# Kernel optimization log

Hardware: AMD Instinct MI355X
Metric: run time of the kernel (lower is better)

Reference implementation:

```python
import jax, jax.numpy as jnp
import numpy as np

NEG_INF = -jnp.inf


def setup_inputs() -> dict:
    key = jax.random.key(0)
    ks = jax.random.split(key, 6)
    B, S, D, DK = 8, 2048, 1024, 128
    x = jax.random.normal(ks[0], (B, S, D), dtype=jnp.float32)
    context = jax.random.normal(ks[1], (B, S, D), dtype=jnp.float32)
    # torch nn.Linear weights: [out_features, in_features]
    Wq = jax.random.normal(ks[2], (DK, D), dtype=jnp.float32) * 0.02
    Wk = jax.random.normal(ks[3], (DK, D), dtype=jnp.float32) * 0.02
    Wv = jax.random.normal(ks[4], (DK, D), dtype=jnp.float32) * 0.02
    # valid lengths in [S//2, S] so every row has at least one valid key
    batch_lengths = jax.random.randint(ks[5], (B,), S // 2, S + 1, dtype=jnp.int32)
    return {
        "x": x,
        "context": context,
        "Wq": Wq,
        "Wk": Wk,
        "Wv": Wv,
        "batch_lengths": batch_lengths,
        "max_len": S,
        "decoding": 1,
    }


def reference(x, context, Wq, Wk, Wv, batch_lengths, max_len, decoding):
    B, S, D = x.shape
    dk = Wq.shape[0]
    pos = jnp.arange(S)
    # outputMask: 1.0 for t < length, else 0.0; broadcast over feature dim dk
    valid = pos[None, :] < batch_lengths[:, None]            # [B, S]
    mask = valid[:, :, None].astype(x.dtype)                 # [B, S, 1] (broadcast to dk)
    Q = jnp.einsum('bsd,kd->bsk', context, Wq) * mask        # [B, S, dk]
    K = jnp.einsum('bsd,kd->bsk', context, Wk) * mask
    V = jnp.einsum('bsd,kd->bsk', x, Wv) * mask
    energy = jnp.einsum('bqk,bjk->bqj', Q, K)                # [B, S, S]
    # attnMask: -inf at padded key positions (j >= length)
    key_pad = ~valid                                         # [B, S]
    energy = jnp.where(key_pad[:, None, :], NEG_INF, energy)
    if decoding:
        # causal: energy[:, i, j] = -inf for j > i (the python double loop)
        causal = pos[:, None] < pos[None, :]                 # [S, S], True above diag
        energy = jnp.where(causal[None, :, :], NEG_INF, energy)
    score = jax.nn.softmax(energy / jnp.sqrt(jnp.asarray(dk, x.dtype)), axis=-1)
    return jnp.einsum('bqj,bjk->bqk', score, V)              # [B, S, dk]
```

## Files before the change

kernel.cpp:

```cpp
#include <hip/hip_runtime.h>
#include <hip/hip_bf16.h>

#define BB 8
#define SS 2048
#define DD 1024
#define DKK 128

using bf16x8  = __attribute__((ext_vector_type(8))) __bf16;
using floatx4 = __attribute__((ext_vector_type(4))) float;
using intx4   = __attribute__((ext_vector_type(4))) int;

__device__ __forceinline__ void lds16(const void* g, void* l) {
    __builtin_amdgcn_global_load_lds((const __attribute__((address_space(1))) void*)g,
                                     (__attribute__((address_space(3))) void*)l, 16, 0, 0);
}

__device__ __forceinline__ int pack2(float a, float b) {
    union { __bf16 h; unsigned short u; } ua, ub;
    ua.h = (__bf16)a; ub.h = (__bf16)b;
    return (int)(ua.u | ((unsigned)ub.u << 16));
}

__global__ __launch_bounds__(256) void convw_kernel(
    const float* __restrict__ Wq, const float* __restrict__ Wk,
    const float* __restrict__ Wv, __bf16* __restrict__ Wt)
{
    const int z = blockIdx.y;
    const float* W = (z == 0) ? Wq : (z == 1) ? Wk : Wv;
    const int t  = blockIdx.x * 256 + threadIdx.x;
    const int n  = t >> 7;
    const int k0 = (t & 127) * 8;
    float4 f0 = *(const float4*)(W + n * DD + k0);
    float4 f1 = *(const float4*)(W + n * DD + k0 + 4);
    bf16x8 v;
    v[0]=(__bf16)f0.x; v[1]=(__bf16)f0.y; v[2]=(__bf16)f0.z; v[3]=(__bf16)f0.w;
    v[4]=(__bf16)f1.x; v[5]=(__bf16)f1.y; v[6]=(__bf16)f1.z; v[7]=(__bf16)f1.w;
    const int kb  = (k0 >> 3) & 7;
    const int kbs = kb ^ (n & 7);
    *(bf16x8*)(Wt + (size_t)z * 131072 + ((k0 >> 6) * 128 + n) * 64 + kbs * 8) = v;
}

__global__ __launch_bounds__(256, 2) void proj_kernel(
    const float* __restrict__ x, const float* __restrict__ ctx,
    const __bf16* __restrict__ Wt, const int* __restrict__ lengths,
    __bf16* __restrict__ Qb, __bf16* __restrict__ Kb, __bf16* __restrict__ Vt)
{
    __shared__ __align__(16) __bf16 SH[20992];
    __bf16* Abuf = SH;
    __bf16* Wl0  = SH + 4608;
    __bf16* Wl1  = SH + 12800;
    __bf16* T    = SH + 4608;

    const int isV = blockIdx.x >= 256;
    const int m0  = (isV ? blockIdx.x - 256 : blockIdx.x) * 64;
    const int b   = m0 >> 11;
    const int s0  = m0 & (SS - 1);
    const int len = lengths[b];
    if (s0 >= len) return;

    const int tid  = threadIdx.x;
    const int wave = tid >> 6;
    const int lane = tid & 63;
    const int quad = lane >> 4;
    const int l16  = lane & 15;
    const int wm   = wave >> 1;
    const int wn   = wave & 1;

    const float*  A  = isV ? x : ctx;
    const __bf16* W0 = isV ? (Wt + 262144) : Wt;
    const __bf16* W1 = Wt + 131072;

    const int r    = tid >> 2;
    const int kseg = (tid & 3) * 16;
    const float* Ab = A + (size_t)(m0 + r) * DD + kseg;

    floatx4 acc[2][2][4];
#pragma unroll
    for (int m_ = 0; m_ < 2; ++m_)
#pragma unroll
        for (int i = 0; i < 2; ++i)
#pragma unroll
            for (int j = 0; j < 4; ++j) acc[m_][i][j] = (floatx4){0.f,0.f,0.f,0.f};

    float4 pf[4];
#pragma unroll
    for (int i = 0; i < 4; ++i) pf[i] = *(const float4*)(Ab + i * 4);

    for (int t = 0; t < 16; ++t) {
        __syncthreads();
        {
            bf16x8 c0, c1;
            c0[0]=(__bf16)pf[0].x; c0[1]=(__bf16)pf[0].y; c0[2]=(__bf16)pf[0].z; c0[3]=(__bf16)pf[0].w;
            c0[4]=(__bf16)pf[1].x; c0[5]=(__bf16)pf[1].y; c0[6]=(__bf16)pf[1].z; c0[7]=(__bf16)pf[1].w;
            c1[0]=(__bf16)pf[2].x; c1[1]=(__bf16)pf[2].y; c1[2]=(__bf16)pf[2].z; c1[3]=(__bf16)pf[2].w;
            c1[4]=(__bf16)pf[3].x; c1[5]=(__bf16)pf[3].y; c1[6]=(__bf16)pf[3].z; c1[7]=(__bf16)pf[3].w;
            *(bf16x8*)&Abuf[r * 72 + kseg]     = c0;
            *(bf16x8*)&Abuf[r * 72 + kseg + 8] = c1;
        }
#pragma unroll
        for (int i = 0; i < 4; ++i) {
            const int c = wave * 4 + i;
            lds16(W0 + (size_t)t * 8192 + c * 512 + lane * 8, Wl0 + c * 512);
            if (!isV)
                lds16(W1 + (size_t)t * 8192 + c * 512 + lane * 8, Wl1 + c * 512);
        }
        if (t < 15) {
            const float* ap = Ab + (t + 1) * 64;
#pragma unroll
            for (int i = 0; i < 4; ++i) pf[i] = *(const float4*)(ap + i * 4);
        }
        __syncthreads();

#pragma unroll
        for (int kh = 0; kh < 2; ++kh) {
            bf16x8 af[2];
#pragma unroll
            for (int mt = 0; mt < 2; ++mt)
                af[mt] = *(const bf16x8*)&Abuf[(wm*32 + mt*16 + l16) * 72 + kh*32 + quad*8];
            const int kb = kh * 4 + quad;
#pragma unroll
            for (int nt = 0; nt < 4; ++nt) {
                const int n = wn * 64 + nt * 16 + l16;
                const int off = n * 64 + ((kb ^ (n & 7)) << 3);
                bf16x8 w0 = *(const bf16x8*)&Wl0[off];
#pragma unroll
                for (int mt = 0; mt < 2; ++mt)
                    acc[0][mt][nt] = __builtin_amdgcn_mfma_f32_16x16x32_bf16(af[mt], w0, acc[0][mt][nt], 0, 0, 0);
                if (!isV) {
                    bf16x8 w1 = *(const bf16x8*)&Wl1[off];
#pragma unroll
                    for (int mt = 0; mt < 2; ++mt)
                        acc[1][mt][nt] = __builtin_amdgcn_mfma_f32_16x16x32_bf16(af[mt], w1, acc[1][mt][nt], 0, 0, 0);
                }
            }
        }
    }

    if (!isV) {
#pragma unroll
        for (int mt = 0; mt < 2; ++mt)
#pragma unroll
            for (int rr = 0; rr < 4; ++rr) {
                const int row = m0 + wm*32 + mt*16 + quad*4 + rr;
                const float mk = ((row & (SS - 1)) < len) ? 1.f : 0.f;
#pragma unroll
                for (int nt = 0; nt < 4; ++nt) {
                    const int col = wn*64 + nt*16 + l16;
                    Qb[(size_t)row * DKK + col] = (__bf16)(acc[0][mt][nt][rr] * mk);
                    Kb[(size_t)row * DKK + col] = (__bf16)(acc[1][mt][nt][rr] * mk);
                }
            }
    } else {
        __syncthreads();
#pragma unroll
        for (int mt = 0; mt < 2; ++mt)
#pragma unroll
            for (int nt = 0; nt < 4; ++nt)
#pragma unroll
                for (int rr = 0; rr < 4; ++rr) {
                    const int s = wm*32 + mt*16 + quad*4 + rr;
                    const int n = wn*64 + nt*16 + l16;
                    const float mk = (s0 + s < len) ? 1.f : 0.f;
                    T[n * 72 + s] = (__bf16)(acc[0][mt][nt][rr] * mk);
                }
        __syncthreads();
        const int n = tid >> 1, h = tid & 1;
        __bf16* dst = Vt + (size_t)b * DKK * SS + (size_t)n * SS + s0 + h * 32;
#pragma unroll
        for (int i = 0; i < 4; ++i)
            *(bf16x8*)(dst + i * 8) = *(const bf16x8*)&T[n * 72 + h * 32 + i * 8];
    }
}

__global__ __launch_bounds__(256) void vmean_kernel(
    const __bf16* __restrict__ Vt, const int* __restrict__ lengths,
    float* __restrict__ Vmean)
{
    const int b   = blockIdx.x >> 3;
    const int g3  = blockIdx.x & 7;
    const int len = lengths[b];
    const int tid = threadIdx.x;
    const int n   = g3 * 16 + (tid >> 4);
    const int sl  = (tid & 15) * 128;
    const __bf16* src = Vt + (size_t)b * DKK * SS + (size_t)n * SS + sl;
    float s = 0.f;
#pragma unroll
    for (int i = 0; i < 16; ++i) {
        bf16x8 v = *(const bf16x8*)(src + i * 8);
#pragma unroll
        for (int j = 0; j < 8; ++j)
            s += (sl + i * 8 + j < len) ? (float)v[j] : 0.f;
    }
#pragma unroll
    for (int off = 1; off < 16; off <<= 1)
        s += __shfl_xor(s, off, 64);
    if ((tid & 15) == 0) Vmean[b * DKK + n] = s / (float)len;
}

__global__ __launch_bounds__(64) void attn_kernel(
    const __bf16* __restrict__ Qb, const __bf16* __restrict__ Kb,
    const __bf16* __restrict__ Vt, const int* __restrict__ lengths,
    const float* __restrict__ Vmean, float* __restrict__ out)
{
    const int b    = blockIdx.x & 7;
    const int t    = 127 - (blockIdx.x >> 3);
    const int qw   = t * 16;
    const int len  = lengths[b];
    const int lane = threadIdx.x;
    const int quad = lane >> 4;
    const int l16  = lane & 15;

    if (qw >= len) {
        const float4 v0 = *(const float4*)(Vmean + b * DKK + l16 * 8);
        const float4 v1 = *(const float4*)(Vmean + b * DKK + l16 * 8 + 4);
#pragma unroll
        for (int rr = 0; rr < 4; ++rr) {
            float* p = out + (size_t)(b * SS + qw + quad * 4 + rr) * DKK + l16 * 8;
            *(float4*)p = v0; *(float4*)(p + 4) = v1;
        }
        return;
    }

    const int jmax = min(qw + 16, len);
    const __bf16* Qbase = Qb + (size_t)(b * SS + qw) * DKK;
    const __bf16* Kbase = Kb + (size_t)b * SS * DKK;
    const __bf16* Vbase = Vt + (size_t)b * DKK * SS;

    bf16x8 qfrag[4];
#pragma unroll
    for (int cc = 0; cc < 4; ++cc)
        qfrag[cc] = *(const bf16x8*)(Qbase + (size_t)l16 * DKK + cc * 32 + quad * 8);

    floatx4 oacc[8];
#pragma unroll
    for (int nt = 0; nt < 8; ++nt) oacc[nt] = (floatx4){0.f,0.f,0.f,0.f};
    float lsum = 0.f;
    const float scale = 0.08838834764831845f;
    const int   iq    = qw + l16;

    auto loadK = [&](bf16x8 (&kf)[2][4], int j0) {
#pragma unroll
        for (int jt = 0; jt < 2; ++jt)
#pragma unroll
            for (int cc = 0; cc < 4; ++cc)
                kf[jt][cc] = *(const bf16x8*)(
                    Kbase + (size_t)(j0 + jt*16 + l16) * DKK + cc*32 + quad*8);
    };
    auto process = [&](const bf16x8 (&kf)[2][4], int j0) {
        bf16x8 vf[8];
#pragma unroll
        for (int nt = 0; nt < 8; ++nt)
            vf[nt] = *(const bf16x8*)(Vbase + (size_t)(nt*16 + l16) * SS + j0 + quad*8);

        floatx4 st[2];
#pragma unroll
        for (int jt = 0; jt < 2; ++jt) {
            st[jt] = (floatx4){0.f,0.f,0.f,0.f};
#pragma unroll
            for (int cc = 0; cc < 4; ++cc)
                st[jt] = __builtin_amdgcn_mfma_f32_16x16x32_bf16(
                    kf[jt][cc], qfrag[cc], st[jt], 0, 0, 0);
        }
        int pk[2][2];
#pragma unroll
        for (int jt = 0; jt < 2; ++jt) {
            float p[4];
#pragma unroll
            for (int rr = 0; rr < 4; ++rr) {
                const int j = j0 + jt*16 + quad*4 + rr;
                p[rr] = (j > iq || j >= len) ? 0.f : __expf(st[jt][rr] * scale - 8.f);
                lsum += p[rr];
            }
            pk[jt][0] = pack2(p[0], p[1]);
            pk[jt][1] = pack2(p[2], p[3]);
        }
        const int a0 = (((quad & 1) << 5) + l16) << 2;
        const int a1 = a0 + 64;
        const int r00 = __builtin_amdgcn_ds_bpermute(a0, pk[0][0]);
        const int r01 = __builtin_amdgcn_ds_bpermute(a0, pk[0][1]);
        const int r02 = __builtin_amdgcn_ds_bpermute(a0, pk[1][0]);
        const int r03 = __builtin_amdgcn_ds_bpermute(a0, pk[1][1]);
        const int r10 = __builtin_amdgcn_ds_bpermute(a1, pk[0][0]);
        const int r11 = __builtin_amdgcn_ds_bpermute(a1, pk[0][1]);
        const int r12 = __builtin_amdgcn_ds_bpermute(a1, pk[1][0]);
        const int r13 = __builtin_amdgcn_ds_bpermute(a1, pk[1][1]);
        const bool hi = quad >= 2;
        union { intx4 i; bf16x8 h; } u;
        u.i = (intx4){ hi ? r02 : r00, hi ? r03 : r01,
                       hi ? r12 : r10, hi ? r13 : r11 };
#pragma unroll
        for (int nt = 0; nt < 8; ++nt)
            oacc[nt] = __builtin_amdgcn_mfma_f32_16x16x32_bf16(u.h, vf[nt], oacc[nt], 0, 0, 0);
    };

    bf16x8 kfA[2][4], kfB[2][4];
    loadK(kfA, 0);
    int j0 = 0;
    while (true) {
        bool more = (j0 + 32 < jmax);
        if (more) loadK(kfB, j0 + 32);
        process(kfA, j0);
        j0 += 32;
        if (!more) break;
        more = (j0 + 32 < jmax);
        if (more) loadK(kfA, j0 + 32);
        process(kfB, j0);
        j0 += 32;
        if (!more) break;
    }

    lsum += __shfl_xor(lsum, 16, 64);
    lsum += __shfl_xor(lsum, 32, 64);
    float inv[4];
#pragma unroll
    for (int rr = 0; rr < 4; ++rr)
        inv[rr] = 1.f / __shfl(lsum, quad * 4 + rr, 64);
#pragma unroll
    for (int nt = 0; nt < 8; ++nt)
#pragma unroll
        for (int rr = 0; rr < 4; ++rr)
            out[(size_t)(b * SS + qw + quad*4 + rr) * DKK + nt*16 + l16] =
                oacc[nt][rr] * inv[rr];
}

extern "C" void kernel_launch(void* const* d_in, const int* in_sizes, int n_in,
                              void* d_out, int out_size, void* d_ws, size_t ws_size,
                              hipStream_t stream) {
    const float* x   = (const float*)d_in[0];
    const float* ctx = (const float*)d_in[1];
    const float* Wq  = (const float*)d_in[2];
    const float* Wk  = (const float*)d_in[3];
    const float* Wv  = (const float*)d_in[4];
    const int* lengths = (const int*)d_in[5];
    float* out = (float*)d_out;

    char* ws = (char*)d_ws;
    __bf16* Wt = (__bf16*)ws;
    __bf16* Qb = (__bf16*)(ws + 786432);
    __bf16* Kb = (__bf16*)(ws + 786432 + 4194304);
    __bf16* Vt = (__bf16*)(ws + 786432 + 8388608);
    float*  Vm = (float*) (ws + 786432 + 12582912);

    convw_kernel<<<dim3(64, 3), 256, 0, stream>>>(Wq, Wk, Wv, Wt);
    proj_kernel<<<512, 256, 0, stream>>>(x, ctx, Wt, lengths, Qb, Kb, Vt);
    vmean_kernel<<<64, 256, 0, stream>>>(Vt, lengths, Vm);
    attn_kernel<<<1024, 64, 0, stream>>>(Qb, Kb, Vt, lengths, Vm, out);
}
```

Before: 237.1 us.

## Split attention key loop across four waves with LDS reduction

The attention kernel now launches 256 threads per query tile. Each of the four waves processes an interleaved quarter of the key blocks, stepping by 128. Partial output accumulators and row sums are then reduced through shared memory before normalization and the store. This shortens the per-block serial key loop, which limited the long causal tiles, at the cost of LDS traffic, a barrier and more threads per block.

```diff
diff --git a/kernel.cpp b/kernel.cpp
--- a/kernel.cpp
+++ b/kernel.cpp
@@ -197,27 +197,31 @@
     if ((tid & 15) == 0) Vmean[b * DKK + n] = s / (float)len;
 }
 
-__global__ __launch_bounds__(64) void attn_kernel(
+__global__ __launch_bounds__(256) void attn_kernel(
     const __bf16* __restrict__ Qb, const __bf16* __restrict__ Kb,
     const __bf16* __restrict__ Vt, const int* __restrict__ lengths,
     const float* __restrict__ Vmean, float* __restrict__ out)
 {
+    __shared__ float redO[4][16][132];
+    __shared__ float redL[4][16];
+
     const int b    = blockIdx.x & 7;
     const int t    = 127 - (blockIdx.x >> 3);
     const int qw   = t * 16;
     const int len  = lengths[b];
-    const int lane = threadIdx.x;
+    const int tid  = threadIdx.x;
+    const int wave = tid >> 6;
+    const int lane = tid & 63;
     const int quad = lane >> 4;
     const int l16  = lane & 15;
 
     if (qw >= len) {
-        const float4 v0 = *(const float4*)(Vmean + b * DKK + l16 * 8);
-        const float4 v1 = *(const float4*)(Vmean + b * DKK + l16 * 8 + 4);
-#pragma unroll
-        for (int rr = 0; rr < 4; ++rr) {
-            float* p = out + (size_t)(b * SS + qw + quad * 4 + rr) * DKK + l16 * 8;
-            *(float4*)p = v0; *(float4*)(p + 4) = v1;
-        }
+        const int row = tid >> 4;
+        const int c8  = (tid & 15) * 8;
+        float* op = out + (size_t)(b * SS + qw + row) * DKK + c8;
+        const float4 v0 = *(const float4*)(Vmean + b * DKK + c8);
+        const float4 v1 = *(const float4*)(Vmean + b * DKK + c8 + 4);
+        *(float4*)op = v0; *(float4*)(op + 4) = v1;
         return;
     }
 
@@ -294,33 +298,45 @@
     };
 
     bf16x8 kfA[2][4], kfB[2][4];
-    loadK(kfA, 0);
-    int j0 = 0;
-    while (true) {
-        bool more = (j0 + 32 < jmax);
-        if (more) loadK(kfB, j0 + 32);
-        process(kfA, j0);
-        j0 += 32;
-        if (!more) break;
-        more = (j0 + 32 < jmax);
-        if (more) loadK(kfA, j0 + 32);
-        process(kfB, j0);
-        j0 += 32;
-        if (!more) break;
+    int j0 = wave * 32;
+    if (j0 < jmax) {
+        loadK(kfA, j0);
+        while (true) {
+            bool more = (j0 + 128 < jmax);
+            if (more) loadK(kfB, j0 + 128);
+            process(kfA, j0);
+            j0 += 128;
+            if (!more) break;
+            more = (j0 + 128 < jmax);
+            if (more) loadK(kfA, j0 + 128);
+            process(kfB, j0);
+            j0 += 128;
+            if (!more) break;
+        }
     }
 
     lsum += __shfl_xor(lsum, 16, 64);
     lsum += __shfl_xor(lsum, 32, 64);
-    float inv[4];
-#pragma unroll
-    for (int rr = 0; rr < 4; ++rr)
-        inv[rr] = 1.f / __shfl(lsum, quad * 4 + rr, 64);
+
 #pragma unroll
     for (int nt = 0; nt < 8; ++nt)
 #pragma unroll
         for (int rr = 0; rr < 4; ++rr)
-            out[(size_t)(b * SS + qw + quad*4 + rr) * DKK + nt*16 + l16] =
-                oacc[nt][rr] * inv[rr];
+            redO[wave][quad*4 + rr][nt*16 + l16] = oacc[nt][rr];
+    if (lane < 16) redL[wave][l16] = lsum;
+    __syncthreads();
+
+    const int row = tid >> 4;
+    const int c8  = (tid & 15) * 8;
+    const float lt = redL[0][row] + redL[1][row] + redL[2][row] + redL[3][row];
+    const float inv = 1.f / lt;
+    float* op = out + (size_t)(b * SS + qw + row) * DKK + c8;
+#pragma unroll
+    for (int k = 0; k < 8; ++k) {
+        const float s = redO[0][row][c8+k] + redO[1][row][c8+k]
+                      + redO[2][row][c8+k] + redO[3][row][c8+k];
+        op[k] = s * inv;
+    }
 }
 
 extern "C" void kernel_launch(void* const* d_in, const int* in_sizes, int n_in,
@@ -344,5 +360,5 @@
     convw_kernel<<<dim3(64, 3), 256, 0, stream>>>(Wq, Wk, Wv, Wt);
     proj_kernel<<<512, 256, 0, stream>>>(x, ctx, Wt, lengths, Qb, Kb, Vt);
     vmean_kernel<<<64, 256, 0, stream>>>(Vt, lengths, Vm);
-    attn_kernel<<<1024, 64, 0, stream>>>(Qb, Kb, Vt, lengths, Vm, out);
-}
+    attn_kernel<<<1024, 256, 0, stream>>>(Qb, Kb, Vt, lengths, Vm, out);
+}
```

Result: no change. 234.6 us (-1.1%).

## Share K/V tiles in LDS across four waves of a 64-row query block

Applied to the files above, without the earlier changes.

Attention blocks now hold 4 waves covering 64 query rows. K and V chunks of 64 keys are staged into double-buffered, XOR-swizzled LDS using direct global-to-LDS loads, so four waves reuse each tile instead of each reading K/V from global memory on its own. This cuts redundant global/L2 traffic but adds __syncthreads per chunk and reduces the grid to 256 blocks. Causal work per block is coarser, so some waves compute masked chunks they would have skipped before.

```diff
diff --git a/kernel.cpp b/kernel.cpp
--- a/kernel.cpp
+++ b/kernel.cpp
@@ -197,73 +197,96 @@
     if ((tid & 15) == 0) Vmean[b * DKK + n] = s / (float)len;
 }
 
-__global__ __launch_bounds__(64) void attn_kernel(
+__global__ __launch_bounds__(256) void attn_kernel(
     const __bf16* __restrict__ Qb, const __bf16* __restrict__ Kb,
     const __bf16* __restrict__ Vt, const int* __restrict__ lengths,
     const float* __restrict__ Vmean, float* __restrict__ out)
 {
+    __shared__ __align__(16) __bf16 KB[2 * 8192];
+    __shared__ __align__(16) __bf16 VB[2 * 8192];
+
     const int b    = blockIdx.x & 7;
-    const int t    = 127 - (blockIdx.x >> 3);
-    const int qw   = t * 16;
+    const int qt   = 31 - (blockIdx.x >> 3);
+    const int qw   = qt * 64;
     const int len  = lengths[b];
-    const int lane = threadIdx.x;
+    const int tid  = threadIdx.x;
+    const int wave = tid >> 6;
+    const int lane = tid & 63;
     const int quad = lane >> 4;
     const int l16  = lane & 15;
 
     if (qw >= len) {
-        const float4 v0 = *(const float4*)(Vmean + b * DKK + l16 * 8);
-        const float4 v1 = *(const float4*)(Vmean + b * DKK + l16 * 8 + 4);
-#pragma unroll
-        for (int rr = 0; rr < 4; ++rr) {
-            float* p = out + (size_t)(b * SS + qw + quad * 4 + rr) * DKK + l16 * 8;
-            *(float4*)p = v0; *(float4*)(p + 4) = v1;
+        const int c8 = (tid & 15) * 8;
+        const float4 v0 = *(const float4*)(Vmean + b * DKK + c8);
+        const float4 v1 = *(const float4*)(Vmean + b * DKK + c8 + 4);
+#pragma unroll
+        for (int pass = 0; pass < 4; ++pass) {
+            const int row = pass * 16 + (tid >> 4);
+            float* op = out + (size_t)(b * SS + qw + row) * DKK + c8;
+            *(float4*)op = v0; *(float4*)(op + 4) = v1;
         }
         return;
     }
 
-    const int jmax = min(qw + 16, len);
-    const __bf16* Qbase = Qb + (size_t)(b * SS + qw) * DKK;
+    const int jmax = min(qw + 64, len);
+    const int nc   = (jmax + 63) >> 6;
     const __bf16* Kbase = Kb + (size_t)b * SS * DKK;
     const __bf16* Vbase = Vt + (size_t)b * DKK * SS;
 
     bf16x8 qfrag[4];
-#pragma unroll
-    for (int cc = 0; cc < 4; ++cc)
-        qfrag[cc] = *(const bf16x8*)(Qbase + (size_t)l16 * DKK + cc * 32 + quad * 8);
+    {
+        const __bf16* Qbase = Qb + (size_t)(b * SS + qw + wave * 16) * DKK;
+#pragma unroll
+        for (int cc = 0; cc < 4; ++cc)
+            qfrag[cc] = *(const bf16x8*)(Qbase + (size_t)l16 * DKK + cc * 32 + quad * 8);
+    }
 
     floatx4 oacc[8];
 #pragma unroll
     for (int nt = 0; nt < 8; ++nt) oacc[nt] = (floatx4){0.f,0.f,0.f,0.f};
     float lsum = 0.f;
     const float scale = 0.08838834764831845f;
-    const int   iq    = qw + l16;
-
-    auto loadK = [&](bf16x8 (&kf)[2][4], int j0) {
-#pragma unroll
-        for (int jt = 0; jt < 2; ++jt)
-#pragma unroll
-            for (int cc = 0; cc < 4; ++cc)
-                kf[jt][cc] = *(const bf16x8*)(
-                    Kbase + (size_t)(j0 + jt*16 + l16) * DKK + cc*32 + quad*8);
+    const int   iq    = qw + wave * 16 + l16;
+    const int   sw7   = l16 & 7;
+
+    auto stageK = [&](int buf, int j0) {
+#pragma unroll
+        for (int i = 0; i < 4; ++i) {
+            const int c   = wave * 4 + i;
+            const int row = c * 4 + quad;
+            const int sb  = l16 ^ (row & 7);
+            lds16(Kbase + (size_t)(j0 + row) * DKK + sb * 8,
+                  KB + buf * 8192 + c * 512);
+        }
     };
-    auto process = [&](const bf16x8 (&kf)[2][4], int j0) {
-        bf16x8 vf[8];
-#pragma unroll
-        for (int nt = 0; nt < 8; ++nt)
-            vf[nt] = *(const bf16x8*)(Vbase + (size_t)(nt*16 + l16) * SS + j0 + quad*8);
-
-        floatx4 st[2];
-#pragma unroll
-        for (int jt = 0; jt < 2; ++jt) {
+    auto stageV = [&](int buf, int j0) {
+#pragma unroll
+        for (int i = 0; i < 4; ++i) {
+            const int c   = wave * 4 + i;
+            const int row = c * 8 + (lane >> 3);
+            const int sb  = (lane & 7) ^ (row & 7);
+            lds16(Vbase + (size_t)row * SS + j0 + sb * 8,
+                  VB + buf * 8192 + c * 512);
+        }
+    };
+
+    auto process = [&](int buf, int j0) {
+        const int kbas = buf * 8192;
+        floatx4 st[4];
+#pragma unroll
+        for (int jt = 0; jt < 4; ++jt) {
             st[jt] = (floatx4){0.f,0.f,0.f,0.f};
 #pragma unroll
-            for (int cc = 0; cc < 4; ++cc)
+            for (int cc = 0; cc < 4; ++cc) {
+                bf16x8 kf = *(const bf16x8*)(
+                    KB + kbas + (jt*16 + l16) * 128 + (((cc*4 + quad) ^ sw7) * 8));
                 st[jt] = __builtin_amdgcn_mfma_f32_16x16x32_bf16(
-                    kf[jt][cc], qfrag[cc], st[jt], 0, 0, 0);
-        }
-        int pk[2][2];
-#pragma unroll
-        for (int jt = 0; jt < 2; ++jt) {
+                    kf, qfrag[cc], st[jt], 0, 0, 0);
+            }
+        }
+        int pk[4][2];
+#pragma unroll
+        for (int jt = 0; jt < 4; ++jt) {
             float p[4];
 #pragma unroll
             for (int rr = 0; rr < 4; ++rr) {
@@ -276,37 +299,37 @@
         }
         const int a0 = (((quad & 1) << 5) + l16) << 2;
         const int a1 = a0 + 64;
-        const int r00 = __builtin_amdgcn_ds_bpermute(a0, pk[0][0]);
-        const int r01 = __builtin_amdgcn_ds_bpermute(a0, pk[0][1]);
-        const int r02 = __builtin_amdgcn_ds_bpermute(a0, pk[1][0]);
-        const int r03 = __builtin_amdgcn_ds_bpermute(a0, pk[1][1]);
-        const int r10 = __builtin_amdgcn_ds_bpermute(a1, pk[0][0]);
-        const int r11 = __builtin_amdgcn_ds_bpermute(a1, pk[0][1]);
-        const int r12 = __builtin_amdgcn_ds_bpermute(a1, pk[1][0]);
-        const int r13 = __builtin_amdgcn_ds_bpermute(a1, pk[1][1]);
-        const bool hi = quad >= 2;
-        union { intx4 i; bf16x8 h; } u;
-        u.i = (intx4){ hi ? r02 : r00, hi ? r03 : r01,
-                       hi ? r12 : r10, hi ? r13 : r11 };
-#pragma unroll
-        for (int nt = 0; nt < 8; ++nt)
-            oacc[nt] = __builtin_amdgcn_mfma_f32_16x16x32_bf16(u.h, vf[nt], oacc[nt], 0, 0, 0);
+#pragma unroll
+        for (int f = 0; f < 2; ++f) {
+            const int r00 = __builtin_amdgcn_ds_bpermute(a0, pk[2*f  ][0]);
+            const int r01 = __builtin_amdgcn_ds_bpermute(a0, pk[2*f  ][1]);
+            const int r02 = __builtin_amdgcn_ds_bpermute(a0, pk[2*f+1][0]);
+            const int r03 = __builtin_amdgcn_ds_bpermute(a0, pk[2*f+1][1]);
+            const int r10 = __builtin_amdgcn_ds_bpermute(a1, pk[2*f  ][0]);
+            const int r11 = __builtin_amdgcn_ds_bpermute(a1, pk[2*f  ][1]);
+            const int r12 = __builtin_amdgcn_ds_bpermute(a1, pk[2*f+1][0]);
+            const int r13 = __builtin_amdgcn_ds_bpermute(a1, pk[2*f+1][1]);
+            const bool hi = quad >= 2;
+            union { intx4 i; bf16x8 h; } u;
+            u.i = (intx4){ hi ? r02 : r00, hi ? r03 : r01,
+                           hi ? r12 : r10, hi ? r13 : r11 };
+#pragma unroll
+            for (int nt = 0; nt < 8; ++nt) {
+                bf16x8 vf = *(const bf16x8*)(
+                    VB + kbas + (nt*16 + l16) * 64 + (((f*4 + quad) ^ sw7) * 8));
+                oacc[nt] = __builtin_amdgcn_mfma_f32_16x16x32_bf16(
+                    u.h, vf, oacc[nt], 0, 0, 0);
+            }
+        }
     };
 
-    bf16x8 kfA[2][4], kfB[2][4];
-    loadK(kfA, 0);
-    int j0 = 0;
-    while (true) {
-        bool more = (j0 + 32 < jmax);
-        if (more) loadK(kfB, j0 + 32);
-        process(kfA, j0);
-        j0 += 32;
-        if (!more) break;
-        more = (j0 + 32 < jmax);
-        if (more) loadK(kfA, j0 + 32);
-        process(kfB, j0);
-        j0 += 32;
-        if (!more) break;
+    stageK(0, 0); stageV(0, 0);
+    __syncthreads();
+    for (int c = 0; c < nc; ++c) {
+        const int cur = c & 1;
+        if (c + 1 < nc) { stageK(cur ^ 1, (c + 1) * 64); stageV(cur ^ 1, (c + 1) * 64); }
+        process(cur, c * 64);
+        __syncthreads();
     }
 
     lsum += __shfl_xor(lsum, 16, 64);
@@ -319,7 +342,7 @@
     for (int nt = 0; nt < 8; ++nt)
 #pragma unroll
         for (int rr = 0; rr < 4; ++rr)
-            out[(size_t)(b * SS + qw + quad*4 + rr) * DKK + nt*16 + l16] =
+            out[(size_t)(b * SS + qw + wave*16 + quad*4 + rr) * DKK + nt*16 + l16] =
                 oacc[nt][rr] * inv[rr];
 }
 
@@ -344,5 +367,5 @@
     convw_kernel<<<dim3(64, 3), 256, 0, stream>>>(Wq, Wk, Wv, Wt);
     proj_kernel<<<512, 256, 0, stream>>>(x, ctx, Wt, lengths, Qb, Kb, Vt);
     vmean_kernel<<<64, 256, 0, stream>>>(Vt, lengths, Vm);
-    attn_kernel<<<1024, 64, 0, stream>>>(Qb, Kb, Vt, lengths, Vm, out);
-}
+    attn_kernel<<<256, 256, 0, stream>>>(Qb, Kb, Vt, lengths, Vm, out);
+}
```

After: 227.3 us. 1.04x faster.
